# Kernel optimization log

Hardware: AMD Instinct MI355X
Metric: run time of the kernel (lower is better)

Reference implementation:

```python
import jax, jax.numpy as jnp
import numpy as np

LN_EPS = 1e-5  # torch LayerNorm default


def setup_inputs() -> dict:
    key = jax.random.key(0)
    ks = jax.random.split(key, 6)
    N, E, D = 50000, 800000, 128
    x = jax.random.normal(ks[0], (N, D), dtype=jnp.float32)
    edge_index = jax.random.randint(ks[1], (2, E), 0, N, dtype=jnp.int64)
    # Linear params (torch default-ish init scale)
    W = jax.random.normal(ks[2], (D, D), dtype=jnp.float32) / np.sqrt(D)
    b = jax.random.normal(ks[3], (D,), dtype=jnp.float32) * 0.01
    # LayerNorm params
    gamma = jnp.ones((D,), dtype=jnp.float32)
    beta = jnp.zeros((D,), dtype=jnp.float32)
    return {"x": x, "edge_index": edge_index, "W": W, "b": b,
            "gamma": gamma, "beta": beta}


def reference(x, edge_index, W, b, gamma, beta):
    N = x.shape[0]
    # add_self_loops
    loops = jnp.arange(N, dtype=edge_index.dtype)
    row = jnp.concatenate([edge_index[0], loops])  # sources (x_j)
    col = jnp.concatenate([edge_index[1], loops])  # targets (aggregate here)

    h = x @ W.T + b  # [N, D]

    # symmetric normalization: deg computed on row, includes self loops (deg>=1)
    deg = jax.ops.segment_sum(jnp.ones(row.shape, dtype=h.dtype), row,
                              num_segments=N)
    dis = deg ** -0.5
    norm = dis[row] * dis[col]  # [E+N]

    # gather-scale-scatter message passing (aggr='add')
    msg = norm[:, None] * h[row]              # [E+N, D]
    agg = jax.ops.segment_sum(msg, col, num_segments=N)  # [N, D]

    out = jax.nn.relu(agg)
    # dropout: identity (eval mode)
    mu = jnp.mean(out, axis=-1, keepdims=True)
    var = jnp.var(out, axis=-1, keepdims=True)
    out = (out - mu) * jax.lax.rsqrt(var + LN_EPS) * gamma + beta
    return out + x  # residual (in_channels == out_channels, no proj)
```

## Files before the change

### kernel.cpp

```cpp
#include <hip/hip_runtime.h>


#define D 128
#define CHSH 15
#define CHUNK (1 << CHSH)
#define NWORD 12500

typedef short bf16x8 __attribute__((ext_vector_type(8)));
typedef float f32x4 __attribute__((ext_vector_type(4)));

__device__ __forceinline__ unsigned short f2bf(float f) {
    unsigned u = __float_as_uint(f);
    return (unsigned short)((u + 0x7fffu + ((u >> 16) & 1u)) >> 16);
}
__device__ __forceinline__ float bf2f_lo(unsigned v) { return __uint_as_float(v << 16); }
__device__ __forceinline__ float bf2f_hi(unsigned v) { return __uint_as_float(v & 0xffff0000u); }

__global__ void k_cast4(const float4* __restrict__ src, ushort4* __restrict__ dst, int n4) {
    int i = blockIdx.x * 256 + threadIdx.x;
    if (i < n4) {
        float4 v = src[i];
        ushort4 o;
        o.x = f2bf(v.x); o.y = f2bf(v.y); o.z = f2bf(v.z); o.w = f2bf(v.w);
        dst[i] = o;
    }
}

__global__ void __launch_bounds__(1024)
k_gemm_hist(const float* __restrict__ x, const unsigned short* __restrict__ wb,
            const float* __restrict__ bias, unsigned short* __restrict__ hb,
            int nrows,
            const int* __restrict__ ei, int E, int n,
            unsigned char* __restrict__ degc, unsigned char* __restrict__ cntc,
            unsigned char* __restrict__ aux, int K) {
    __shared__ unsigned hist[NWORD];
    int bid = blockIdx.x;
    if (bid < 2 * K) {
        bool is_cnt = bid < K;
        int c = is_cnt ? bid : bid - K;
        const int* vs = is_cnt ? (ei + E) : ei;
        for (int i = threadIdx.x; i < NWORD; i += 1024) hist[i] = 0u;
        __syncthreads();
        int e0 = c << CHSH;
        int e1 = e0 + CHUNK; if (e1 > E) e1 = E;
        if (is_cnt) {
            for (int e = e0 + threadIdx.x; e < e1; e += 1024) {
                int v = vs[e];
                unsigned sh = (v & 3) * 8;
                unsigned old = atomicAdd(&hist[v >> 2], 1u << sh);
                aux[e] = (unsigned char)(old >> sh);
            }
        } else {
            for (int e = e0 + threadIdx.x; e < e1; e += 1024) {
                int v = vs[e];
                atomicAdd(&hist[v >> 2], 1u << ((v & 3) * 8));
            }
        }
        __syncthreads();
        unsigned* dst = (unsigned*)((is_cnt ? cntc : degc) + (size_t)c * n);
        for (int i = threadIdx.x; i < NWORD; i += 1024) dst[i] = hist[i];
    } else {
        int wid = threadIdx.x >> 6, lane = threadIdx.x & 63;
        int m0 = (bid - 2 * K) * 256 + wid * 16;
        if (m0 >= nrows) return;
        int lo16 = lane & 15, quad = lane >> 4;
        const float* arow = x + (size_t)(m0 + lo16) * D + quad * 8;
        bf16x8 a[4];
        #pragma unroll
        for (int kt = 0; kt < 4; kt++) {
            float4 p = *(const float4*)(arow + kt * 32);
            float4 q = *(const float4*)(arow + kt * 32 + 4);
            bf16x8 av;
            av[0] = (short)f2bf(p.x); av[1] = (short)f2bf(p.y);
            av[2] = (short)f2bf(p.z); av[3] = (short)f2bf(p.w);
            av[4] = (short)f2bf(q.x); av[5] = (short)f2bf(q.y);
            av[6] = (short)f2bf(q.z); av[7] = (short)f2bf(q.w);
            a[kt] = av;
        }
        #pragma unroll
        for (int nt = 0; nt < 8; nt++) {
            int n0 = nt * 16;
            const unsigned short* brow = wb + (size_t)(n0 + lo16) * D + quad * 8;
            float bj = bias[n0 + lo16];
            f32x4 acc = {bj, bj, bj, bj};
            #pragma unroll
            for (int kt = 0; kt < 4; kt++) {
                bf16x8 b = *(const bf16x8*)(brow + kt * 32);
                acc = __builtin_amdgcn_mfma_f32_16x16x32_bf16(a[kt], b, acc, 0, 0, 0);
            }
            #pragma unroll
            for (int r = 0; r < 4; r++) {
                int gr = m0 + quad * 4 + r;
                hb[(size_t)gr * D + n0 + lo16] = f2bf(acc[r]);
            }
        }
    }
}

__global__ void k_partial(const unsigned char* __restrict__ degc,
                          const unsigned char* __restrict__ cntc,
                          float* __restrict__ dis, unsigned* __restrict__ cnt,
                          unsigned* __restrict__ partial, int n, int K) {
    __shared__ unsigned s[256];
    int t = threadIdx.x;
    int i = blockIdx.x * 256 + t;
    unsigned tot = 0;
    if (i < n) {
        unsigned d = 0;
        for (int c = 0; c < K; c++) d += degc[(size_t)c * n + i];
        dis[i] = rsqrtf((float)d + 1.0f);
        for (int c = 0; c < K; c++) tot += cntc[(size_t)c * n + i];
        cnt[i] = tot;
    }
    s[t] = tot;
    __syncthreads();
    #pragma unroll
    for (int d = 128; d > 0; d >>= 1) {
        if (t < d) s[t] += s[t + d];
        __syncthreads();
    }
    if (t == 0) partial[blockIdx.x] = s[0];
}

__global__ void k_scanp(unsigned* __restrict__ partial, int nb) {
    __shared__ unsigned s[256];
    int t = threadIdx.x;
    unsigned v = (t < nb) ? partial[t] : 0u;
    s[t] = v;
    __syncthreads();
    #pragma unroll
    for (int d = 1; d < 256; d <<= 1) {
        unsigned u = (t >= d) ? s[t - d] : 0u;
        __syncthreads();
        s[t] += u;
        __syncthreads();
    }
    if (t < nb) partial[t] = s[t] - v;
}

__global__ void k_rowptrc(const unsigned* __restrict__ cnt, const unsigned char* __restrict__ cntc,
                          const unsigned* __restrict__ partial, int n, int E,
                          int* __restrict__ rowptr, int* __restrict__ rowptrc, int K) {
    __shared__ unsigned s[256];
    int t = threadIdx.x;
    int i = blockIdx.x * 256 + t;
    unsigned v = (i < n) ? cnt[i] : 0u;
    s[t] = v;
    __syncthreads();
    #pragma unroll
    for (int d = 1; d < 256; d <<= 1) {
        unsigned u = (t >= d) ? s[t - d] : 0u;
        __syncthreads();
        s[t] += u;
        __syncthreads();
    }
    if (i < n) {
        int base = (int)(partial[blockIdx.x] + s[t] - v);
        rowptr[i] = base;
        unsigned run = 0;
        for (int c = 0; c < K; c++) {
            rowptrc[(size_t)c * n + i] = base + (int)run;
            run += cntc[(size_t)c * n + i];
        }
    }
    if (blockIdx.x == 0 && t == 0) rowptr[n] = E;
}

__global__ void k_fill(const int* __restrict__ ei, int E, int n,
                       const int* __restrict__ rowptrc, const unsigned char* __restrict__ aux,
                       int* __restrict__ srcs) {
    int e = blockIdx.x * 256 + threadIdx.x;
    if (e < E) {
        int r = ei[e];
        int v = ei[E + e];
        int c = e >> CHSH;
        srcs[rowptrc[(size_t)c * n + v] + (int)aux[e]] = r;
    }
}

__global__ void k_agg(const float* __restrict__ x, const unsigned short* __restrict__ hb,
                      const float* __restrict__ dis,
                      const int* __restrict__ rowptr, const int* __restrict__ srcs,
                      const float* __restrict__ gamma, const float* __restrict__ beta,
                      float* __restrict__ out, int n) {
    int wid = threadIdx.x >> 6, lane = threadIdx.x & 63;
    int row = blockIdx.x * 4 + wid;
    if (row >= n) return;
    int q = lane >> 4, t = lane & 15;
    float dc = dis[row];
    float acc[8];
    #pragma unroll
    for (int i = 0; i < 8; i++) acc[i] = 0.0f;
    if (q == 0) {
        uint4 u = ((const uint4*)(hb + (size_t)row * D))[t];
        float sn = dc * dc;
        acc[0] = sn * bf2f_lo(u.x); acc[1] = sn * bf2f_hi(u.x);
        acc[2] = sn * bf2f_lo(u.y); acc[3] = sn * bf2f_hi(u.y);
        acc[4] = sn * bf2f_lo(u.z); acc[5] = sn * bf2f_hi(u.z);
        acc[6] = sn * bf2f_lo(u.w); acc[7] = sn * bf2f_hi(u.w);
    }
    int s0 = rowptr[row];
    int len = rowptr[row + 1] - s0;
    for (int base = 0; base < len; base += 64) {
        int idx = base + lane;
        int sv = (idx < len) ? srcs[s0 + idx] : 0;
        float dv = (idx < len) ? dis[sv] : 0.0f;
        int m = len - base; if (m > 64) m = 64;
        int kmax = (m + 3) >> 2;
        int j = q;
        int r = __shfl(sv, j, 64);
        float nm = dc * __shfl(dv, j, 64);
        uint4 u = ((const uint4*)(hb + (size_t)r * D))[t];
        for (int k = 1; k < kmax; k++) {
            int jn = j + 4;
            int rn = __shfl(sv, jn, 64);
            float nmn = dc * __shfl(dv, jn, 64);
            uint4 un = ((const uint4*)(hb + (size_t)rn * D))[t];
            acc[0] += nm * bf2f_lo(u.x); acc[1] += nm * bf2f_hi(u.x);
            acc[2] += nm * bf2f_lo(u.y); acc[3] += nm * bf2f_hi(u.y);
            acc[4] += nm * bf2f_lo(u.z); acc[5] += nm * bf2f_hi(u.z);
            acc[6] += nm * bf2f_lo(u.w); acc[7] += nm * bf2f_hi(u.w);
            u = un; nm = nmn; j = jn;
        }
        acc[0] += nm * bf2f_lo(u.x); acc[1] += nm * bf2f_hi(u.x);
        acc[2] += nm * bf2f_lo(u.y); acc[3] += nm * bf2f_hi(u.y);
        acc[4] += nm * bf2f_lo(u.z); acc[5] += nm * bf2f_hi(u.z);
        acc[6] += nm * bf2f_lo(u.w); acc[7] += nm * bf2f_hi(u.w);
    }
    #pragma unroll
    for (int i = 0; i < 8; i++) {
        acc[i] += __shfl_xor(acc[i], 16, 64);
        acc[i] += __shfl_xor(acc[i], 32, 64);
        acc[i] = acc[i] > 0.0f ? acc[i] : 0.0f;
    }
    float s1r = 0.0f, s2r = 0.0f;
    #pragma unroll
    for (int i = 0; i < 8; i++) { s1r += acc[i]; s2r += acc[i] * acc[i]; }
    #pragma unroll
    for (int mm = 8; mm >= 1; mm >>= 1) {
        s1r += __shfl_xor(s1r, mm, 64);
        s2r += __shfl_xor(s2r, mm, 64);
    }
    float mean = s1r * (1.0f / 128.0f);
    float var  = s2r * (1.0f / 128.0f) - mean * mean;
    float rstd = rsqrtf(var + 1e-5f);
    if (q == 0) {
        const float4* gr = (const float4*)gamma;
        const float4* br = (const float4*)beta;
        const float4* xr = (const float4*)(x + (size_t)row * D);
        float4* orow = (float4*)(out + (size_t)row * D);
        #pragma unroll
        for (int hf = 0; hf < 2; hf++) {
            float4 g = gr[2 * t + hf], b = br[2 * t + hf], xx = xr[2 * t + hf];
            float4 o;
            o.x = (acc[4 * hf + 0] - mean) * rstd * g.x + b.x + xx.x;
            o.y = (acc[4 * hf + 1] - mean) * rstd * g.y + b.y + xx.y;
            o.z = (acc[4 * hf + 2] - mean) * rstd * g.z + b.z + xx.z;
            o.w = (acc[4 * hf + 3] - mean) * rstd * g.w + b.w + xx.w;
            orow[2 * t + hf] = o;
        }
    }
}

extern "C" void kernel_launch(void* const* d_in, const int* in_sizes, int n_in,
                              void* d_out, int out_size, void* d_ws, size_t ws_size,
                              hipStream_t stream) {
    const float* x     = (const float*)d_in[0];
    const int*   ei    = (const int*)d_in[1];
    const float* W     = (const float*)d_in[2];
    const float* bias  = (const float*)d_in[3];
    const float* gamma = (const float*)d_in[4];
    const float* beta  = (const float*)d_in[5];
    int N = in_sizes[0] / D;
    int E = in_sizes[1] / 2;
    int nb  = (N + 255) / 256;
    int nbE = (E + 255) / 256;
    int K   = (E + CHUNK - 1) >> CHSH;
    int gemm_blocks = (N + 255) / 256;

    char* ws = (char*)d_ws;
    size_t off = 0;
    unsigned short* hb  = (unsigned short*)(ws + off); off += (size_t)N * D * 2;
    unsigned short* wbf = (unsigned short*)(ws + off); off += (size_t)D * D * 2;
    unsigned char* degc = (unsigned char*)(ws + off);  off += (size_t)K * N;
    unsigned char* cntc = (unsigned char*)(ws + off);  off += (size_t)K * N;
    float*    dis       = (float*)(ws + off);          off += (size_t)N * 4;
    unsigned* cnt       = (unsigned*)(ws + off);       off += (size_t)N * 4;
    int*      rowptr    = (int*)(ws + off);            off += (size_t)(N + 1) * 4;
    int*      rowptrc   = (int*)(ws + off);            off += (size_t)K * N * 4;
    unsigned* partial   = (unsigned*)(ws + off);       off += 256 * 4;
    unsigned char* aux  = (unsigned char*)(ws + off);  off += (size_t)E;
    int*      srcs      = (int*)(ws + off);            off += (size_t)E * 4;
    float*    out       = (float*)d_out;

    k_cast4<<<(D * D / 4 + 255) / 256, 256, 0, stream>>>((const float4*)W, (ushort4*)wbf, D * D / 4);
    k_gemm_hist<<<2 * K + gemm_blocks, 1024, 0, stream>>>(x, wbf, bias, hb, N,
                                                          ei, E, N, degc, cntc, aux, K);
    k_partial<<<nb, 256, 0, stream>>>(degc, cntc, dis, cnt, partial, N, K);
    k_scanp<<<1, 256, 0, stream>>>(partial, nb);
    k_rowptrc<<<nb, 256, 0, stream>>>(cnt, cntc, partial, N, E, rowptr, rowptrc, K);
    k_fill<<<nbE, 256, 0, stream>>>(ei, E, N, rowptrc, aux, srcs);
    k_agg<<<(N + 3) / 4, 256, 0, stream>>>(x, hb, dis, rowptr, srcs, gamma, beta, out, N);
}
```

Measured before the change: 183.2 us.

## Fuse three-pass CSR prefix scan into single-pass decoupled look-back scan

Replaces the partial-sum, block-scan and rowptr kernels with one kernel that computes per-block totals and resolves block offsets through decoupled look-back on global flags. Flags are zeroed in the weight-cast kernel. This removes two launches and the intermediate count/partial arrays and their re-reads of the per-chunk counters. In exchange it relies on blocks being scheduled roughly in order, and serial spinning on predecessor flags could add latency.

Result: slower. 220.1 us (+20.1%).

```diff
diff --git a/kernel.cpp b/kernel.cpp
--- a/kernel.cpp
+++ b/kernel.cpp
@@ -16,8 +16,10 @@
 __device__ __forceinline__ float bf2f_lo(unsigned v) { return __uint_as_float(v << 16); }
 __device__ __forceinline__ float bf2f_hi(unsigned v) { return __uint_as_float(v & 0xffff0000u); }
 
-__global__ void k_cast4(const float4* __restrict__ src, ushort4* __restrict__ dst, int n4) {
+__global__ void k_cast4(const float4* __restrict__ src, ushort4* __restrict__ dst, int n4,
+                        unsigned* __restrict__ flags) {
     int i = blockIdx.x * 256 + threadIdx.x;
+    if (blockIdx.x == 0) flags[threadIdx.x] = 0u;
     if (i < n4) {
         float4 v = src[i];
         ushort4 o;
@@ -97,73 +99,63 @@
     }
 }
 
-__global__ void k_partial(const unsigned char* __restrict__ degc,
-                          const unsigned char* __restrict__ cntc,
-                          float* __restrict__ dis, unsigned* __restrict__ cnt,
-                          unsigned* __restrict__ partial, int n, int K) {
+__global__ void k_scan(const unsigned char* __restrict__ degc,
+                       const unsigned char* __restrict__ cntc,
+                       float* __restrict__ dis,
+                       int* __restrict__ rowptr, int* __restrict__ rowptrc,
+                       unsigned* __restrict__ flags, int n, int E, int K) {
     __shared__ unsigned s[256];
+    __shared__ unsigned sbase;
     int t = threadIdx.x;
-    int i = blockIdx.x * 256 + t;
+    int bid = blockIdx.x;
+    int i = bid * 256 + t;
     unsigned tot = 0;
     if (i < n) {
         unsigned d = 0;
         for (int c = 0; c < K; c++) d += degc[(size_t)c * n + i];
         dis[i] = rsqrtf((float)d + 1.0f);
         for (int c = 0; c < K; c++) tot += cntc[(size_t)c * n + i];
-        cnt[i] = tot;
     }
     s[t] = tot;
     __syncthreads();
     #pragma unroll
-    for (int d = 128; d > 0; d >>= 1) {
-        if (t < d) s[t] += s[t + d];
-        __syncthreads();
-    }
-    if (t == 0) partial[blockIdx.x] = s[0];
-}
-
-__global__ void k_scanp(unsigned* __restrict__ partial, int nb) {
-    __shared__ unsigned s[256];
-    int t = threadIdx.x;
-    unsigned v = (t < nb) ? partial[t] : 0u;
-    s[t] = v;
-    __syncthreads();
-    #pragma unroll
     for (int d = 1; d < 256; d <<= 1) {
         unsigned u = (t >= d) ? s[t - d] : 0u;
         __syncthreads();
         s[t] += u;
         __syncthreads();
     }
-    if (t < nb) partial[t] = s[t] - v;
-}
-
-__global__ void k_rowptrc(const unsigned* __restrict__ cnt, const unsigned char* __restrict__ cntc,
-                          const unsigned* __restrict__ partial, int n, int E,
-                          int* __restrict__ rowptr, int* __restrict__ rowptrc, int K) {
-    __shared__ unsigned s[256];
-    int t = threadIdx.x;
-    int i = blockIdx.x * 256 + t;
-    unsigned v = (i < n) ? cnt[i] : 0u;
-    s[t] = v;
+    unsigned incl = s[t];
+    unsigned aggregate = s[255];
+    if (t == 0) {
+        __hip_atomic_store(&flags[bid], (1u << 30) | aggregate,
+                           __ATOMIC_RELEASE, __HIP_MEMORY_SCOPE_AGENT);
+        unsigned ex = 0;
+        for (int p = bid - 1; p >= 0; p--) {
+            unsigned f;
+            do {
+                f = __hip_atomic_load(&flags[p], __ATOMIC_ACQUIRE,
+                                      __HIP_MEMORY_SCOPE_AGENT);
+            } while ((f >> 30) == 0u);
+            ex += f & 0x3FFFFFFFu;
+            if ((f >> 30) == 2u) break;
+        }
+        __hip_atomic_store(&flags[bid], (2u << 30) | (ex + aggregate),
+                           __ATOMIC_RELEASE, __HIP_MEMORY_SCOPE_AGENT);
+        sbase = ex;
+    }
     __syncthreads();
-    #pragma unroll
-    for (int d = 1; d < 256; d <<= 1) {
-        unsigned u = (t >= d) ? s[t - d] : 0u;
-        __syncthreads();
-        s[t] += u;
-        __syncthreads();
-    }
+    unsigned base = sbase;
     if (i < n) {
-        int base = (int)(partial[blockIdx.x] + s[t] - v);
-        rowptr[i] = base;
+        int rb = (int)(base + incl - tot);
+        rowptr[i] = rb;
         unsigned run = 0;
         for (int c = 0; c < K; c++) {
-            rowptrc[(size_t)c * n + i] = base + (int)run;
+            rowptrc[(size_t)c * n + i] = rb + (int)run;
             run += cntc[(size_t)c * n + i];
         }
     }
-    if (blockIdx.x == 0 && t == 0) rowptr[n] = E;
+    if (i == n - 1) rowptr[n] = E;
 }
 
 __global__ void k_fill(const int* __restrict__ ei, int E, int n,
@@ -285,20 +277,18 @@
     unsigned char* degc = (unsigned char*)(ws + off);  off += (size_t)K * N;
     unsigned char* cntc = (unsigned char*)(ws + off);  off += (size_t)K * N;
     float*    dis       = (float*)(ws + off);          off += (size_t)N * 4;
-    unsigned* cnt       = (unsigned*)(ws + off);       off += (size_t)N * 4;
     int*      rowptr    = (int*)(ws + off);            off += (size_t)(N + 1) * 4;
     int*      rowptrc   = (int*)(ws + off);            off += (size_t)K * N * 4;
-    unsigned* partial   = (unsigned*)(ws + off);       off += 256 * 4;
+    unsigned* flags     = (unsigned*)(ws + off);       off += 256 * 4;
     unsigned char* aux  = (unsigned char*)(ws + off);  off += (size_t)E;
     int*      srcs      = (int*)(ws + off);            off += (size_t)E * 4;
     float*    out       = (float*)d_out;
 
-    k_cast4<<<(D * D / 4 + 255) / 256, 256, 0, stream>>>((const float4*)W, (ushort4*)wbf, D * D / 4);
+    k_cast4<<<(D * D / 4 + 255) / 256, 256, 0, stream>>>((const float4*)W, (ushort4*)wbf,
+                                                         D * D / 4, flags);
     k_gemm_hist<<<2 * K + gemm_blocks, 1024, 0, stream>>>(x, wbf, bias, hb, N,
                                                           ei, E, N, degc, cntc, aux, K);
-    k_partial<<<nb, 256, 0, stream>>>(degc, cntc, dis, cnt, partial, N, K);
-    k_scanp<<<1, 256, 0, stream>>>(partial, nb);
-    k_rowptrc<<<nb, 256, 0, stream>>>(cnt, cntc, partial, N, E, rowptr, rowptrc, K);
+    k_scan<<<nb, 256, 0, stream>>>(degc, cntc, dis, rowptr, rowptrc, flags, N, E, K);
     k_fill<<<nbE, 256, 0, stream>>>(ei, E, N, rowptrc, aux, srcs);
     k_agg<<<(N + 3) / 4, 256, 0, stream>>>(x, hb, dis, rowptr, srcs, gamma, beta, out, N);
 }
```
